# Optimization experiments

Hardware: AMD Instinct MI355X
Metric: run time of the kernel (lower is better)

## Reference

```python
import jax, jax.numpy as jnp
import numpy as np

N_NODES = 100_000
DEG = 16
N_EDGES = N_NODES * DEG
NODE_F = 128
EDGE_F = 16
HID = 64
B = 64
K = DEG


def setup_inputs() -> dict:
    key = jax.random.key(0)
    ks = jax.random.split(key, 12)
    # node i's outgoing edges are at ids i + k*N_NODES for k in [0, DEG)
    src = jnp.arange(N_EDGES, dtype=jnp.int32) % N_NODES
    dst = jax.random.randint(ks[0], (N_EDGES,), 0, N_NODES, dtype=jnp.int32)
    edge_index = jnp.stack([src, dst])
    current_nodes = jax.random.randint(ks[1], (B,), 0, N_NODES, dtype=jnp.int32)
    # reachable neighbors = destinations of the current node's real edges
    neighbor_nodes = dst[current_nodes[:, None] + jnp.arange(K, dtype=jnp.int32)[None, :] * N_NODES]
    x = jax.random.normal(ks[2], (N_NODES, NODE_F), jnp.float32)
    edge_attr = jax.random.normal(ks[3], (N_EDGES, EDGE_F), jnp.float32)
    return dict(
        x=x,
        edge_attr=edge_attr,
        conv1_W=jax.random.normal(ks[4], (NODE_F, HID), jnp.float32) * (NODE_F ** -0.5),
        conv1_b=jnp.zeros((HID,), jnp.float32),
        conv2_W=jax.random.normal(ks[5], (HID, HID), jnp.float32) * (HID ** -0.5),
        conv2_b=jnp.zeros((HID,), jnp.float32),
        mlp_W1=jax.random.normal(ks[6], (2 * HID + EDGE_F, 2 * HID), jnp.float32) * ((2 * HID + EDGE_F) ** -0.5),
        mlp_b1=jnp.zeros((2 * HID,), jnp.float32),
        mlp_W2=jax.random.normal(ks[7], (2 * HID, 1), jnp.float32) * ((2 * HID) ** -0.5),
        mlp_b2=jnp.zeros((1,), jnp.float32),
        edge_index=edge_index,
        current_nodes=current_nodes,
        neighbor_nodes=neighbor_nodes,
    )


def gcn_conv(x, edge_index, W, b):
    """PyG GCNConv: symmetric norm with self-loops, then linear + bias."""
    n = x.shape[0]
    loop = jnp.arange(n, dtype=edge_index.dtype)
    src = jnp.concatenate([edge_index[0], loop])  # messages flow src -> dst
    dst = jnp.concatenate([edge_index[1], loop])
    xw = x @ W                                    # [N, H]
    deg = jnp.zeros((n,), xw.dtype).at[dst].add(1.0)
    dinv = jnp.where(deg > 0, jax.lax.rsqrt(deg), 0.0)
    msg = (dinv[src] * dinv[dst])[:, None] * xw[src]      # [E+N, H]
    return jax.ops.segment_sum(msg, dst, num_segments=n) + b


def reference(x, edge_attr, conv1_W, conv1_b, conv2_W, conv2_b,
              mlp_W1, mlp_b1, mlp_W2, mlp_b2,
              edge_index, current_nodes, neighbor_nodes):
    n = x.shape[0]
    h = jax.nn.relu(gcn_conv(x, edge_index, conv1_W, conv1_b))
    h = jax.nn.relu(gcn_conv(h, edge_index, conv2_W, conv2_b))

    # First edge id matching each (current, neighbor) pair, replacing the
    # original O(E)-per-neighbor boolean-mask loop with a sorted-key lookup.
    keys = edge_index[0].astype(jnp.int64) * n + edge_index[1].astype(jnp.int64)
    order = jnp.argsort(keys, stable=True)        # stable -> leftmost == first edge id
    skeys = keys[order]
    query = current_nodes[:, None].astype(jnp.int64) * n + neighbor_nodes.astype(jnp.int64)
    pos = jnp.clip(jnp.searchsorted(skeys, query), 0, skeys.shape[0] - 1)
    valid = skeys[pos] == query                   # [B, K]
    eid = order[pos]
    ea = edge_attr[eid]                           # [B, K, F]

    b_, k_ = neighbor_nodes.shape
    h_cur = jnp.broadcast_to(h[current_nodes][:, None, :], (b_, k_, h.shape[1]))
    h_nbr = h[neighbor_nodes]
    m = jnp.concatenate([h_cur, h_nbr, ea], axis=-1)  # [B, K, 2H+F]
    q = (jax.nn.relu(m @ mlp_W1 + mlp_b1) @ mlp_W2 + mlp_b2)[..., 0]
    q = jnp.where(valid, q, 0.0)
    return q, valid
```

## Files before the change

### kernel.cpp

```cpp
#include <hip/hip_runtime.h>

#define N_NODES 100000
#define DEG 16
#define N_EDGES (N_NODES * DEG)
#define NODE_F 128
#define EDGE_F 16
#define HID 64
#define NQ 1024
#define NCHUNK (N_EDGES / 256)
#define XTILES ((N_NODES + 63) / 64)
#define NHIST 4096
#define BCAP 56
#define NDINV ((N_NODES + 255) / 256)
#define MAGIC 0x13579BDF

__global__ void k_query_zero(const int* __restrict__ dst, const int* __restrict__ cur,
                             const int* __restrict__ nbr, int* __restrict__ n1,
                             int* __restrict__ n2, int* __restrict__ wcur,
                             int* __restrict__ eid_sel, float* __restrict__ out_valid,
                             int* __restrict__ degp) {
  if (blockIdx.x >= 4) {
    int4* d4 = (int4*)degp;
    const int n4 = 8 * N_NODES / 4;
    int i = (blockIdx.x - 4) * 256 + threadIdx.x;
    const int stride = (gridDim.x - 4) * 256;
    for (; i < n4; i += stride) d4[i] = make_int4(0, 0, 0, 0);
    return;
  }
  int i = blockIdx.x * 256 + threadIdx.x;
  if (i >= NQ) return;
  int b = i >> 4;
  int c = cur[b];
  int nb = nbr[i];
  int sel = -1;
  #pragma unroll
  for (int j = 0; j < DEG; ++j) {
    int e = c + j * N_NODES;
    if (sel < 0 && dst[e] == nb) sel = e;
  }
  eid_sel[i] = sel;
  out_valid[i] = (sel >= 0) ? 1.0f : 0.0f;
  n2[c] = MAGIC; n2[nb] = MAGIC;
  n1[c] = MAGIC; n1[nb] = MAGIC;
  wcur[c] = 0;   wcur[nb] = 0;
}

__global__ __launch_bounds__(256) void k_fusedA(
    const float* __restrict__ x, const float* __restrict__ Wg,
    float* __restrict__ xw, const int* __restrict__ dst,
    const int* __restrict__ n2, int* __restrict__ n1, int* __restrict__ wcur,
    int* __restrict__ degp) {
  __shared__ float xs[64 * 129];
  const int t = threadIdx.x;

  if (blockIdx.x < NHIST) {
    int* __restrict__ dp = degp + (size_t)(blockIdx.x & 7) * N_NODES;
    for (int e = blockIdx.x * 256 + t; e < N_EDGES; e += NHIST * 256) {
      int d = dst[e];
      atomicAdd(&dp[d], 1);
      if (n2[d] == MAGIC) {
        int s = e % N_NODES;
        n1[s] = MAGIC;
        wcur[s] = 0;
      }
    }
    return;
  }

  const int lane = t & 63;
  const int w = __builtin_amdgcn_readfirstlane(t >> 6);
  const long base = (long)(blockIdx.x - NHIST) * 64;

  const float4* __restrict__ xv = (const float4*)x;
  #pragma unroll
  for (int p = 0; p < 8; ++p) {
    int f4 = p * 256 + t;
    int r = f4 >> 5;
    int c4 = f4 & 31;
    long gr = base + r;
    float4 v = make_float4(0.f, 0.f, 0.f, 0.f);
    if (gr < N_NODES) v = xv[gr * 32 + c4];
    float* d = &xs[r * 129 + (c4 << 2)];
    d[0] = v.x; d[1] = v.y; d[2] = v.z; d[3] = v.w;
  }
  __syncthreads();

  float acc[16];
  #pragma unroll
  for (int j = 0; j < 16; ++j) acc[j] = 0.f;
  const float* __restrict__ wp = Wg + w * 16;
  #pragma unroll 4
  for (int k = 0; k < NODE_F; ++k) {
    float xk = xs[lane * 129 + k];
    float wv[16];
    #pragma unroll
    for (int j = 0; j < 16; ++j) wv[j] = wp[k * HID + j];
    #pragma unroll
    for (int j = 0; j < 16; ++j) acc[j] = fmaf(xk, wv[j], acc[j]);
  }
  long gr = base + lane;
  if (gr < N_NODES) {
    float* __restrict__ op = xw + gr * HID + w * 16;
    #pragma unroll
    for (int j = 0; j < 16; ++j) op[j] = acc[j];
  }
}

__global__ void k_bucket_dinv(const int* __restrict__ dst, const int* __restrict__ n1,
                              int* __restrict__ wcur, int* __restrict__ bucket,
                              const int* __restrict__ degp, float* __restrict__ dinv) {
  if (blockIdx.x < NDINV) {
    int v = blockIdx.x * 256 + threadIdx.x;
    if (v < N_NODES) {
      int s = 1;
      #pragma unroll
      for (int p = 0; p < 8; ++p) s += degp[(size_t)p * N_NODES + v];
      dinv[v] = rsqrtf((float)s);
    }
    return;
  }
  int e = (blockIdx.x - NDINV) * 256 + threadIdx.x;
  int d = dst[e];
  if (n1[d] != MAGIC) return;
  int pos = atomicAdd(&wcur[d], 1);
  if (pos >= 0 && pos < BCAP)
    bucket[(size_t)d * BCAP + pos] = e % N_NODES;
}

__global__ void k_xw2(const float* __restrict__ h1, const float* __restrict__ Wg,
                      const int* __restrict__ n1, float* __restrict__ xw2) {
  const int lane = threadIdx.x & 63;
  const int row = (blockIdx.x * blockDim.x + threadIdx.x) >> 6;
  if (row >= N_NODES) return;
  if (n1[row] != MAGIC) return;
  const float* __restrict__ hr = h1 + (size_t)row * HID;
  float acc = 0.f;
  #pragma unroll
  for (int k = 0; k < HID; ++k) acc = fmaf(hr[k], Wg[k * HID + lane], acc);
  xw2[(size_t)row * HID + lane] = acc;
}

__global__ __launch_bounds__(256) void k_gather(
    const int* __restrict__ bucket, const int* __restrict__ wcur,
    const int* __restrict__ flag, const float* __restrict__ dinv,
    const float* __restrict__ xw, const float* __restrict__ bias,
    float* __restrict__ hout) {
  const int t = threadIdx.x;
  const int lane = t & 63;
  const int v = blockIdx.x * 4 + (t >> 6);
  if (v >= N_NODES) return;
  if (flag[v] != MAGIC) return;
  int n = wcur[v];
  if (n > BCAP) n = BCAP;
  if (n < 0) n = 0;
  int   s_l = (lane < n) ? bucket[(size_t)v * BCAP + lane] : 0;
  float w_l = (lane < n) ? dinv[s_l] : 0.f;
  float acc = 0.f;
  int j = 0;
  for (; j + 3 < n; j += 4) {
    int s0 = __shfl(s_l, j);
    int s1 = __shfl(s_l, j + 1);
    int s2 = __shfl(s_l, j + 2);
    int s3 = __shfl(s_l, j + 3);
    float a0 = xw[(size_t)s0 * HID + lane];
    float a1 = xw[(size_t)s1 * HID + lane];
    float a2 = xw[(size_t)s2 * HID + lane];
    float a3 = xw[(size_t)s3 * HID + lane];
    acc = fmaf(__shfl(w_l, j), a0, acc);
    acc = fmaf(__shfl(w_l, j + 1), a1, acc);
    acc = fmaf(__shfl(w_l, j + 2), a2, acc);
    acc = fmaf(__shfl(w_l, j + 3), a3, acc);
  }
  for (; j < n; ++j)
    acc = fmaf(__shfl(w_l, j), xw[(size_t)__shfl(s_l, j) * HID + lane], acc);
  float dv = dinv[v];
  acc = fmaf(dv, xw[(size_t)v * HID + lane], acc);
  hout[(size_t)v * HID + lane] = fmaxf(fmaf(dv, acc, bias[lane]), 0.f);
}

__global__ void k_mlp(const float* __restrict__ h2, const float* __restrict__ ea,
                      const float* __restrict__ W1, const float* __restrict__ b1,
                      const float* __restrict__ W2, const float* __restrict__ b2,
                      const int* __restrict__ cur, const int* __restrict__ nbr,
                      const int* __restrict__ eid_sel, float* __restrict__ out) {
  __shared__ float m[2 * HID + EDGE_F];
  __shared__ float red[128];
  const int q = blockIdx.x;
  const int t = threadIdx.x;
  const int eid = eid_sel[q];
  if (eid < 0) {
    if (t == 0) out[q] = 0.0f;
    return;
  }
  const int b = q >> 4;
  const int c = cur[b];
  const int nb = nbr[q];
  if (t < HID)    m[t] = h2[(size_t)c * HID + t];
  else            m[t] = h2[(size_t)nb * HID + (t - HID)];
  if (t < EDGE_F) m[2 * HID + t] = ea[(size_t)eid * EDGE_F + t];
  __syncthreads();
  float h = b1[t];
  #pragma unroll
  for (int j = 0; j < 2 * HID + EDGE_F; ++j) h = fmaf(m[j], W1[j * 128 + t], h);
  h = fmaxf(h, 0.f) * W2[t];
  red[t] = h;
  __syncthreads();
  if (t < 64) {
    float v = red[t] + red[t + 64];
    #pragma unroll
    for (int o = 32; o > 0; o >>= 1) v += __shfl_down(v, o);
    if (t == 0) out[q] = v + b2[0];
  }
}

extern "C" void kernel_launch(void* const* d_in, const int* in_sizes, int n_in,
                              void* d_out, int out_size, void* d_ws, size_t ws_size,
                              hipStream_t stream) {
  const float* x    = (const float*)d_in[0];
  const float* ea   = (const float*)d_in[1];
  const float* c1W  = (const float*)d_in[2];
  const float* c1b  = (const float*)d_in[3];
  const float* c2W  = (const float*)d_in[4];
  const float* c2b  = (const float*)d_in[5];
  const float* mW1  = (const float*)d_in[6];
  const float* mb1  = (const float*)d_in[7];
  const float* mW2  = (const float*)d_in[8];
  const float* mb2  = (const float*)d_in[9];
  const int*   eidx = (const int*)d_in[10];
  const int*   cur  = (const int*)d_in[11];
  const int*   nbr  = (const int*)d_in[12];
  const int* edst = eidx + N_EDGES;
  float* out = (float*)d_out;

  char* p = (char*)d_ws;
  auto alloc = [&](size_t bytes) -> void* {
    void* r = (void*)p;
    p += (bytes + 255) & ~(size_t)255;
    return r;
  };
  int*   degp    = (int*)alloc((size_t)8 * N_NODES * 4);
  float* dinv    = (float*)alloc((size_t)N_NODES * 4);
  int*   n1      = (int*)alloc((size_t)N_NODES * 4);
  int*   n2      = (int*)alloc((size_t)N_NODES * 4);
  int*   wcur    = (int*)alloc((size_t)N_NODES * 4);
  int*   eid_sel = (int*)alloc((size_t)NQ * 4);
  int*   bucket  = (int*)alloc((size_t)N_NODES * BCAP * 4);
  float* xw1     = (float*)alloc((size_t)N_NODES * HID * 4);
  float* h1      = (float*)alloc((size_t)N_NODES * HID * 4);
  float* xw2     = (float*)alloc((size_t)N_NODES * HID * 4);
  float* h2      = xw1;

  k_query_zero<<<260, 256, 0, stream>>>(edst, cur, nbr, n1, n2, wcur, eid_sel,
                                        out + NQ, degp);
  k_fusedA<<<NHIST + XTILES, 256, 0, stream>>>(x, c1W, xw1, edst, n2, n1, wcur,
                                               degp);
  k_bucket_dinv<<<NDINV + NCHUNK, 256, 0, stream>>>(edst, n1, wcur, bucket, degp,
                                                    dinv);
  k_gather<<<(N_NODES + 3) / 4, 256, 0, stream>>>(bucket, wcur, n1, dinv, xw1,
                                                  c1b, h1);
  k_xw2<<<(N_NODES * HID + 255) / 256, 256, 0, stream>>>(h1, c2W, n1, xw2);
  k_gather<<<(N_NODES + 3) / 4, 256, 0, stream>>>(bucket, wcur, n2, dinv, xw2,
                                                  c2b, h2);
  k_mlp<<<NQ, 128, 0, stream>>>(h2, ea, mW1, mb1, mW2, mb2, cur, nbr, eid_sel, out);
}
```

Baseline: 361.9 us.

## Fuse layer-1 gather with conv2 matmul, XCC-local degree histograms, swizzled x tile

Merges the first-layer GCN gather with the second-layer linear transform into one kernel, which drops the h1 buffer and a kernel launch. The degree histogram copy is now picked by the hardware XCC id, its atomics use workgroup scope, and the histogram block count is halved. The x tile in LDS switches from padding to an XOR swizzle, and the weight loads and output stores use float4. Workgroup-scope atomics on a per-XCC copy rely on all blocks of one XCC sharing an L2, which is a correctness risk if that assumption does not hold.

New measurement: 354.9 us. About the same (-1.9%).

```diff
diff --git a/kernel.cpp b/kernel.cpp
--- a/kernel.cpp
+++ b/kernel.cpp
@@ -9,10 +9,16 @@
 #define NQ 1024
 #define NCHUNK (N_EDGES / 256)
 #define XTILES ((N_NODES + 63) / 64)
-#define NHIST 4096
+#define NHIST 2048
 #define BCAP 56
 #define NDINV ((N_NODES + 255) / 256)
 #define MAGIC 0x13579BDF
+
+__device__ __forceinline__ int xcc_id() {
+  int x;
+  asm("s_getreg_b32 %0, hwreg(HW_REG_XCC_ID)" : "=s"(x));
+  return x & 7;
+}
 
 __global__ void k_query_zero(const int* __restrict__ dst, const int* __restrict__ cur,
                              const int* __restrict__ nbr, int* __restrict__ n1,
@@ -50,14 +56,16 @@
     float* __restrict__ xw, const int* __restrict__ dst,
     const int* __restrict__ n2, int* __restrict__ n1, int* __restrict__ wcur,
     int* __restrict__ degp) {
-  __shared__ float xs[64 * 129];
+  __shared__ float xs[64 * 128];
   const int t = threadIdx.x;
 
   if (blockIdx.x < NHIST) {
-    int* __restrict__ dp = degp + (size_t)(blockIdx.x & 7) * N_NODES;
-    for (int e = blockIdx.x * 256 + t; e < N_EDGES; e += NHIST * 256) {
+    int* __restrict__ dp = degp + (size_t)xcc_id() * N_NODES;
+    const int stride = NHIST * 256;
+    for (int e = blockIdx.x * 256 + t; e < N_EDGES; e += stride) {
       int d = dst[e];
-      atomicAdd(&dp[d], 1);
+      __hip_atomic_fetch_add(&dp[d], 1, __ATOMIC_RELAXED,
+                             __HIP_MEMORY_SCOPE_WORKGROUP);
       if (n2[d] == MAGIC) {
         int s = e % N_NODES;
         n1[s] = MAGIC;
@@ -78,31 +86,46 @@
     int r = f4 >> 5;
     int c4 = f4 & 31;
     long gr = base + r;
-    float4 v = make_float4(0.f, 0.f, 0.f, 0.f);
-    if (gr < N_NODES) v = xv[gr * 32 + c4];
-    float* d = &xs[r * 129 + (c4 << 2)];
-    d[0] = v.x; d[1] = v.y; d[2] = v.z; d[3] = v.w;
+    float4 v = (gr < N_NODES) ? xv[gr * 32 + c4]
+                              : make_float4(0.f, 0.f, 0.f, 0.f);
+    int rs = r & 31;
+    float* xr = xs + r * 128;
+    xr[((c4 << 2) + 0) ^ rs] = v.x;
+    xr[((c4 << 2) + 1) ^ rs] = v.y;
+    xr[((c4 << 2) + 2) ^ rs] = v.z;
+    xr[((c4 << 2) + 3) ^ rs] = v.w;
   }
   __syncthreads();
 
   float acc[16];
   #pragma unroll
   for (int j = 0; j < 16; ++j) acc[j] = 0.f;
-  const float* __restrict__ wp = Wg + w * 16;
+  const int ls = lane & 31;
+  const float* __restrict__ xrow = xs + lane * 128;
+  const float4* __restrict__ wp = (const float4*)(Wg + w * 16);
   #pragma unroll 4
   for (int k = 0; k < NODE_F; ++k) {
-    float xk = xs[lane * 129 + k];
-    float wv[16];
-    #pragma unroll
-    for (int j = 0; j < 16; ++j) wv[j] = wp[k * HID + j];
-    #pragma unroll
-    for (int j = 0; j < 16; ++j) acc[j] = fmaf(xk, wv[j], acc[j]);
+    float xk = xrow[k ^ ls];
+    float4 w0 = wp[k * 16 + 0];
+    float4 w1 = wp[k * 16 + 1];
+    float4 w2 = wp[k * 16 + 2];
+    float4 w3 = wp[k * 16 + 3];
+    acc[ 0] = fmaf(xk, w0.x, acc[ 0]); acc[ 1] = fmaf(xk, w0.y, acc[ 1]);
+    acc[ 2] = fmaf(xk, w0.z, acc[ 2]); acc[ 3] = fmaf(xk, w0.w, acc[ 3]);
+    acc[ 4] = fmaf(xk, w1.x, acc[ 4]); acc[ 5] = fmaf(xk, w1.y, acc[ 5]);
+    acc[ 6] = fmaf(xk, w1.z, acc[ 6]); acc[ 7] = fmaf(xk, w1.w, acc[ 7]);
+    acc[ 8] = fmaf(xk, w2.x, acc[ 8]); acc[ 9] = fmaf(xk, w2.y, acc[ 9]);
+    acc[10] = fmaf(xk, w2.z, acc[10]); acc[11] = fmaf(xk, w2.w, acc[11]);
+    acc[12] = fmaf(xk, w3.x, acc[12]); acc[13] = fmaf(xk, w3.y, acc[13]);
+    acc[14] = fmaf(xk, w3.z, acc[14]); acc[15] = fmaf(xk, w3.w, acc[15]);
   }
   long gr = base + lane;
   if (gr < N_NODES) {
-    float* __restrict__ op = xw + gr * HID + w * 16;
-    #pragma unroll
-    for (int j = 0; j < 16; ++j) op[j] = acc[j];
+    float4* __restrict__ op = (float4*)(xw + gr * HID + w * 16);
+    op[0] = make_float4(acc[0], acc[1], acc[2], acc[3]);
+    op[1] = make_float4(acc[4], acc[5], acc[6], acc[7]);
+    op[2] = make_float4(acc[8], acc[9], acc[10], acc[11]);
+    op[3] = make_float4(acc[12], acc[13], acc[14], acc[15]);
   }
 }
 
@@ -127,17 +150,47 @@
     bucket[(size_t)d * BCAP + pos] = e % N_NODES;
 }
 
-__global__ void k_xw2(const float* __restrict__ h1, const float* __restrict__ Wg,
-                      const int* __restrict__ n1, float* __restrict__ xw2) {
-  const int lane = threadIdx.x & 63;
-  const int row = (blockIdx.x * blockDim.x + threadIdx.x) >> 6;
-  if (row >= N_NODES) return;
-  if (n1[row] != MAGIC) return;
-  const float* __restrict__ hr = h1 + (size_t)row * HID;
+__global__ __launch_bounds__(256) void k_gather_xw2(
+    const int* __restrict__ bucket, const int* __restrict__ wcur,
+    const int* __restrict__ n1, const float* __restrict__ dinv,
+    const float* __restrict__ xw, const float* __restrict__ bias,
+    const float* __restrict__ W2g, float* __restrict__ xw2) {
+  const int t = threadIdx.x;
+  const int lane = t & 63;
+  const int v = blockIdx.x * 4 + (t >> 6);
+  if (v >= N_NODES) return;
+  if (n1[v] != MAGIC) return;
+  int n = wcur[v];
+  if (n > BCAP) n = BCAP;
+  if (n < 0) n = 0;
+  int   s_l = (lane < n) ? bucket[(size_t)v * BCAP + lane] : 0;
+  float w_l = (lane < n) ? dinv[s_l] : 0.f;
   float acc = 0.f;
-  #pragma unroll
-  for (int k = 0; k < HID; ++k) acc = fmaf(hr[k], Wg[k * HID + lane], acc);
-  xw2[(size_t)row * HID + lane] = acc;
+  int j = 0;
+  for (; j + 3 < n; j += 4) {
+    int s0 = __shfl(s_l, j);
+    int s1 = __shfl(s_l, j + 1);
+    int s2 = __shfl(s_l, j + 2);
+    int s3 = __shfl(s_l, j + 3);
+    float a0 = xw[(size_t)s0 * HID + lane];
+    float a1 = xw[(size_t)s1 * HID + lane];
+    float a2 = xw[(size_t)s2 * HID + lane];
+    float a3 = xw[(size_t)s3 * HID + lane];
+    acc = fmaf(__shfl(w_l, j), a0, acc);
+    acc = fmaf(__shfl(w_l, j + 1), a1, acc);
+    acc = fmaf(__shfl(w_l, j + 2), a2, acc);
+    acc = fmaf(__shfl(w_l, j + 3), a3, acc);
+  }
+  for (; j < n; ++j)
+    acc = fmaf(__shfl(w_l, j), xw[(size_t)__shfl(s_l, j) * HID + lane], acc);
+  float dv = dinv[v];
+  acc = fmaf(dv, xw[(size_t)v * HID + lane], acc);
+  float h = fmaxf(fmaf(dv, acc, bias[lane]), 0.f);
+  float a2s = 0.f;
+  #pragma unroll
+  for (int f = 0; f < HID; ++f)
+    a2s = fmaf(__shfl(h, f), W2g[f * HID + lane], a2s);
+  xw2[(size_t)v * HID + lane] = a2s;
 }
 
 __global__ __launch_bounds__(256) void k_gather(
@@ -246,7 +299,6 @@
   int*   eid_sel = (int*)alloc((size_t)NQ * 4);
   int*   bucket  = (int*)alloc((size_t)N_NODES * BCAP * 4);
   float* xw1     = (float*)alloc((size_t)N_NODES * HID * 4);
-  float* h1      = (float*)alloc((size_t)N_NODES * HID * 4);
   float* xw2     = (float*)alloc((size_t)N_NODES * HID * 4);
   float* h2      = xw1;
 
@@ -256,9 +308,8 @@
                                                degp);
   k_bucket_dinv<<<NDINV + NCHUNK, 256, 0, stream>>>(edst, n1, wcur, bucket, degp,
                                                     dinv);
-  k_gather<<<(N_NODES + 3) / 4, 256, 0, stream>>>(bucket, wcur, n1, dinv, xw1,
-                                                  c1b, h1);
-  k_xw2<<<(N_NODES * HID + 255) / 256, 256, 0, stream>>>(h1, c2W, n1, xw2);
+  k_gather_xw2<<<(N_NODES + 3) / 4, 256, 0, stream>>>(bucket, wcur, n1, dinv, xw1,
+                                                      c1b, c2W, xw2);
   k_gather<<<(N_NODES + 3) / 4, 256, 0, stream>>>(bucket, wcur, n2, dinv, xw2,
                                                   c2b, h2);
   k_mlp<<<NQ, 128, 0, stream>>>(h2, ea, mW1, mb1, mW2, mb2, cur, nbr, eid_sel, out);
```
